# Kernel tuning notes

Measured on AMD Instinct MI355X. Metric: run time of the kernel, lower is better.

The kernel has to match this reference:

```python
import jax, jax.numpy as jnp
import numpy as np


def _rotate_half(x):
    x1, x2 = jnp.split(x, 2, axis=-1)
    return jnp.concatenate([-x2, x1], axis=-1)


def _rope_tables(seq_len, head_dim, base=10000.0):
    inv_freq = 1.0 / (base ** (jnp.arange(0, head_dim, 2, dtype=jnp.float32) / head_dim))
    t = jnp.arange(seq_len, dtype=jnp.float32)
    freqs = jnp.outer(t, inv_freq)  # [S, head_dim/2]
    # torch .repeat(...,2) tiles along last dim -> concat
    cos = jnp.concatenate([jnp.cos(freqs), jnp.cos(freqs)], axis=-1)  # [S, head_dim]
    sin = jnp.concatenate([jnp.sin(freqs), jnp.sin(freqs)], axis=-1)
    return cos[None, None], sin[None, None]  # [1,1,S,head_dim]


def setup_inputs() -> dict:
    key = jax.random.key(0)
    ks = jax.random.split(key, 5)
    B, S, D = 2, 2048, 2048
    sd = 1.0 / np.sqrt(D)
    return {
        "x": jax.random.normal(ks[0], (B, S, D), dtype=jnp.float32),
        "Wq": jax.random.normal(ks[1], (D, D), dtype=jnp.float32) * sd,
        "Wk": jax.random.normal(ks[2], (D, D), dtype=jnp.float32) * sd,
        "Wv": jax.random.normal(ks[3], (D, D), dtype=jnp.float32) * sd,
        "Wo": jax.random.normal(ks[4], (D, D), dtype=jnp.float32) * sd,
        "n_heads": 16,
    }


def reference(x, Wq, Wk, Wv, Wo, n_heads):
    B, S, D = x.shape
    hd = D // n_heads
    # projections (torch Linear: x @ W.T)
    def proj(W):
        return (x @ W.T).reshape(B, S, n_heads, hd).transpose(0, 2, 1, 3)  # [B,H,S,hd]
    q, k, v = proj(Wq), proj(Wk), proj(Wv)
    cos, sin = _rope_tables(S, hd)
    q = q * cos + _rotate_half(q) * sin
    k = k * cos + _rotate_half(k) * sin
    scale = 1.0 / np.sqrt(hd)
    scores = jnp.einsum('bhsd,bhtd->bhst', q, k) * scale  # [B,H,S,S]
    causal = jnp.triu(jnp.ones((S, S), dtype=bool), k=1)
    scores = jnp.where(causal[None, None], -jnp.inf, scores)
    attn = jax.nn.softmax(scores, axis=-1)
    out = jnp.einsum('bhst,bhtd->bhsd', attn, v)
    out = out.transpose(0, 2, 1, 3).reshape(B, S, D)
    return out @ Wo.T
```

## Files before the change

kernel.cpp:

```cpp
#include <hip/hip_runtime.h>
#include <hip/hip_bf16.h>
#include <math.h>

typedef __attribute__((ext_vector_type(8))) short bf16x8;
typedef __attribute__((ext_vector_type(4))) float f32x4;

#define GLB_CAST(p) ((const __attribute__((address_space(1))) void*)(p))
#define LDS_CAST(p) ((__attribute__((address_space(3))) void*)(p))

static __device__ __forceinline__ unsigned short bf16_bits(float x) {
    __hip_bfloat16 h = __float2bfloat16(x);
    return *(unsigned short*)&h;
}

__global__ void cvt_all(const float* __restrict__ x,  const float* __restrict__ wq,
                        const float* __restrict__ wk, const float* __restrict__ wv,
                        const float* __restrict__ wo,
                        __hip_bfloat16* __restrict__ xb,  __hip_bfloat16* __restrict__ wqb,
                        __hip_bfloat16* __restrict__ wkb, __hip_bfloat16* __restrict__ wvb,
                        __hip_bfloat16* __restrict__ wob)
{
    const size_t NX = 8388608, NW = 4194304;
    size_t i = ((size_t)blockIdx.x * 256 + threadIdx.x) * 8;
    const float* s; __hip_bfloat16* d; size_t off;
    if (i < NX) { s = x; d = xb; off = i; }
    else {
        size_t k = i - NX;
        const int seg = (int)(k >> 22);
        off = k & (NW - 1);
        s = seg == 0 ? wq : seg == 1 ? wk : seg == 2 ? wv : wo;
        d = seg == 0 ? wqb : seg == 1 ? wkb : seg == 2 ? wvb : wob;
    }
    float4 a = *(const float4*)(s + off);
    float4 b = *(const float4*)(s + off + 4);
    float t[8] = {a.x, a.y, a.z, a.w, b.x, b.y, b.z, b.w};
    union { unsigned short u[8]; uint4 v; } o;
#pragma unroll
    for (int j = 0; j < 8; ++j) o.u[j] = bf16_bits(t[j]);
    *(uint4*)(d + off) = o.v;
}

__global__ __launch_bounds__(256, 2)
void gemm_qkv(const __hip_bfloat16* __restrict__ A,
              const __hip_bfloat16* __restrict__ Wq,
              const __hip_bfloat16* __restrict__ Wk,
              const __hip_bfloat16* __restrict__ Wv,
              __hip_bfloat16* __restrict__ Qo,
              __hip_bfloat16* __restrict__ Ko,
              __hip_bfloat16* __restrict__ Vto)
{
    const int K = 2048;
    __shared__ __hip_bfloat16 As[128 * 32];
    __shared__ __hip_bfloat16 Bs[128 * 32];
    const int tid = threadIdx.x;
    const int w = tid >> 6, l = tid & 63;
    const int sel = blockIdx.y >> 4;
    const __hip_bfloat16* Bt = sel == 0 ? Wq : (sel == 1 ? Wk : Wv);
    const int m0 = blockIdx.x * 128, n0 = (blockIdx.y & 15) * 128;
    const int wr = w >> 1, wc = w & 1;
    const int lr = l & 15, kh = l >> 4;

    f32x4 acc[4][4] = {};

    for (int kt = 0; kt < 64; ++kt) {
        const int kb = kt * 32;
#pragma unroll
        for (int i = 0; i < 2; ++i) {
            const int s = i * 256 + tid;
            const int r = s >> 2, ks = (s & 3) * 8;
            __builtin_amdgcn_global_load_lds(GLB_CAST(A + (size_t)(m0 + r) * K + kb + ks),
                                             LDS_CAST(As + (size_t)(i * 256 + w * 64) * 8),
                                             16, 0, 0);
            __builtin_amdgcn_global_load_lds(GLB_CAST(Bt + (size_t)(n0 + r) * K + kb + ks),
                                             LDS_CAST(Bs + (size_t)(i * 256 + w * 64) * 8),
                                             16, 0, 0);
        }
        __syncthreads();
        bf16x8 af[4], bfr[4];
#pragma unroll
        for (int m = 0; m < 4; ++m)
            af[m] = *(const bf16x8*)(As + (wr * 64 + m * 16 + lr) * 32 + kh * 8);
#pragma unroll
        for (int n = 0; n < 4; ++n)
            bfr[n] = *(const bf16x8*)(Bs + (wc * 64 + n * 16 + lr) * 32 + kh * 8);
#pragma unroll
        for (int m = 0; m < 4; ++m)
#pragma unroll
            for (int n = 0; n < 4; ++n)
                acc[m][n] = __builtin_amdgcn_mfma_f32_16x16x32_bf16(af[m], bfr[n], acc[m][n], 0, 0, 0);
        __syncthreads();
    }

    __hip_bfloat16* Cout = sel == 0 ? Qo : (sel == 1 ? Ko : Vto);
#pragma unroll
    for (int m = 0; m < 4; ++m) {
        const int r0 = m0 + wr * 64 + m * 16 + kh * 4;
#pragma unroll
        for (int n = 0; n < 4; ++n) {
            const int c = n0 + wc * 64 + n * 16 + lr;
#pragma unroll
            for (int j = 0; j < 4; ++j) {
                const int r = r0 + j;
                const float v = acc[m][n][j];
                const int b = r >> 11, sy = r & 2047, h = c >> 7, dd = c & 127;
                if (sel < 2)
                    Cout[((size_t)(b * 16 + h) * 2048 + sy) * 128 + dd] = __float2bfloat16(v);
                else
                    Cout[((size_t)(b * 16 + h) * 128 + dd) * 2048 + sy] = __float2bfloat16(v);
            }
        }
    }
}

__global__ __launch_bounds__(256, 2)
void gemm_o(const __hip_bfloat16* __restrict__ A,
            const __hip_bfloat16* __restrict__ Bt,
            float* __restrict__ Cout)
{
    const int K = 2048;
    __shared__ __hip_bfloat16 As[128 * 32];
    __shared__ __hip_bfloat16 Bs[128 * 32];
    const int tid = threadIdx.x;
    const int w = tid >> 6, l = tid & 63;
    const int m0 = blockIdx.x * 128, n0 = blockIdx.y * 128;
    const int wr = w >> 1, wc = w & 1;
    const int lr = l & 15, kh = l >> 4;

    f32x4 acc[4][4] = {};

    for (int kt = 0; kt < 64; ++kt) {
        const int kb = kt * 32;
#pragma unroll
        for (int i = 0; i < 2; ++i) {
            const int s = i * 256 + tid;
            const int r = s >> 2, ks = (s & 3) * 8;
            __builtin_amdgcn_global_load_lds(GLB_CAST(A + (size_t)(m0 + r) * K + kb + ks),
                                             LDS_CAST(As + (size_t)(i * 256 + w * 64) * 8),
                                             16, 0, 0);
            __builtin_amdgcn_global_load_lds(GLB_CAST(Bt + (size_t)(n0 + r) * K + kb + ks),
                                             LDS_CAST(Bs + (size_t)(i * 256 + w * 64) * 8),
                                             16, 0, 0);
        }
        __syncthreads();
        bf16x8 af[4], bfr[4];
#pragma unroll
        for (int m = 0; m < 4; ++m)
            af[m] = *(const bf16x8*)(As + (wr * 64 + m * 16 + lr) * 32 + kh * 8);
#pragma unroll
        for (int n = 0; n < 4; ++n)
            bfr[n] = *(const bf16x8*)(Bs + (wc * 64 + n * 16 + lr) * 32 + kh * 8);
#pragma unroll
        for (int m = 0; m < 4; ++m)
#pragma unroll
            for (int n = 0; n < 4; ++n)
                acc[m][n] = __builtin_amdgcn_mfma_f32_16x16x32_bf16(af[m], bfr[n], acc[m][n], 0, 0, 0);
        __syncthreads();
    }

#pragma unroll
    for (int m = 0; m < 4; ++m) {
        const int r0 = m0 + wr * 64 + m * 16 + kh * 4;
#pragma unroll
        for (int n = 0; n < 4; ++n) {
            const int c = n0 + wc * 64 + n * 16 + lr;
#pragma unroll
            for (int j = 0; j < 4; ++j)
                Cout[(size_t)(r0 + j) * 2048 + c] = acc[m][n][j];
        }
    }
}

__global__ void rope_qk(__hip_bfloat16* __restrict__ Q, __hip_bfloat16* __restrict__ Kk) {
    const int row = blockIdx.x * 4 + (threadIdx.x >> 6);
    const int j = threadIdx.x & 63;
    const int s = row & 2047;
    const float inv = __expf((float)j * (-0.14391156831212787f));
    float sn, c;
    __sincosf((float)s * inv, &sn, &c);
    const size_t base = (size_t)row * 128;
    float q1 = __bfloat162float(Q[base + j]);
    float q2 = __bfloat162float(Q[base + 64 + j]);
    Q[base + j]      = __float2bfloat16(q1 * c - q2 * sn);
    Q[base + 64 + j] = __float2bfloat16(q2 * c + q1 * sn);
    float k1 = __bfloat162float(Kk[base + j]);
    float k2 = __bfloat162float(Kk[base + 64 + j]);
    Kk[base + j]      = __float2bfloat16(k1 * c - k2 * sn);
    Kk[base + 64 + j] = __float2bfloat16(k2 * c + k1 * sn);
}

__global__ __launch_bounds__(256, 3)
void flash_part(const __hip_bfloat16* __restrict__ Q,
                const __hip_bfloat16* __restrict__ K,
                const __hip_bfloat16* __restrict__ Vt,
                __hip_bfloat16* __restrict__ AO,
                __hip_bfloat16* __restrict__ OP,
                float* __restrict__ ML)
{
    const int bh = blockIdx.x;
    const int u  = blockIdx.y;
    const int tid = threadIdx.x, w = tid >> 6, l = tid & 63;
    const int lr = l & 15, hi = l >> 4;

    int G, part, P;
    if (u < 16)      { G = 12 + (u >> 2);            part = u & 3;   P = 4; }
    else if (u < 28) { int v = u - 16; G = 8 + v / 3; part = v % 3;  P = 3; }
    else if (u < 36) { int v = u - 28; G = 4 + (v >> 1); part = v & 1; P = 2; }
    else             { G = u - 36;                   part = 0;       P = 1; }
    const int nt = 4 * G + 4;
    const int t0 = (part * nt) / P, t1 = ((part + 1) * nt) / P;
    const bool split = (P > 1);
    const int qb = G * 128 + w * 32;
    const int q0 = qb + lr, q1 = qb + 16 + lr;

    const __hip_bfloat16* Qb = Q  + (size_t)bh * 2048 * 128;
    const __hip_bfloat16* Kb = K  + (size_t)bh * 2048 * 128;
    const __hip_bfloat16* Vb = Vt + (size_t)bh * 128 * 2048;

    __shared__ __align__(16) __hip_bfloat16 Ks[2][32 * 128];
    __shared__ __align__(16) __hip_bfloat16 Vs[2][128 * 32];

    bf16x8 qf[2][4];
#pragma unroll
    for (int g = 0; g < 2; ++g)
#pragma unroll
        for (int kk = 0; kk < 4; ++kk)
            qf[g][kk] = *(const bf16x8*)(Qb + (size_t)(qb + g * 16 + lr) * 128 + kk * 32 + hi * 8);

    int rK[2], cK[2], rV[2], cV[2];
#pragma unroll
    for (int i = 0; i < 2; ++i) {
        const int ci = i * 4 + w;
        rK[i] = ci * 4 + (l >> 4);
        cK[i] = ((l & 15) ^ (rK[i] & 7)) * 8;
        rV[i] = ci * 16 + (l >> 2);
        cV[i] = ((l & 3) ^ (rV[i] & 3)) * 8;
    }
    const int rsw7 = lr & 7, vsw3 = lr & 3;
    const int sA = lr + ((hi & 1) << 5);
    const int sB = sA + 16;
    const bool plo = (hi < 2);

#define STAGE(buf, t)                                                                        \
    {                                                                                        \
        const int kv0_ = (t) * 32;                                                           \
        _Pragma("unroll")                                                                    \
        for (int i = 0; i < 2; ++i) {                                                        \
            __builtin_amdgcn_global_load_lds(                                                \
                GLB_CAST(Kb + (size_t)(kv0_ + rK[i]) * 128 + cK[i]),                         \
                LDS_CAST(&Ks[buf][(i * 4 + w) * 512]), 16, 0, 0);                            \
            __builtin_amdgcn_global_load_lds(                                                \
                GLB_CAST(Vb + (size_t)rV[i] * 2048 + kv0_ + cV[i]),                          \
                LDS_CAST(&Vs[buf][(i * 4 + w) * 512]), 16, 0, 0);                            \
        }                                                                                    \
    }

    f32x4 o[2][8] = {};
    float mrow[2] = {-1e30f, -1e30f};
    float lrow[2] = {0.f, 0.f};
    const float scale = 0.08838834764831845f;

    int cur = 0;
    STAGE(0, t0);
    __syncthreads();

    for (int t = t0; t < t1; ++t) {
        if (t + 1 < t1) STAGE(cur ^ 1, t + 1);
        const __hip_bfloat16* Kc = &Ks[cur][0];
        const __hip_bfloat16* Vc = &Vs[cur][0];
        const int kv0 = t * 32;

        f32x4 sT[2][2] = {};
#pragma unroll
        for (int f = 0; f < 2; ++f)
#pragma unroll
            for (int kk = 0; kk < 4; ++kk) {
                const bf16x8 kf = *(const bf16x8*)(Kc + (f * 16 + lr) * 128 +
                                                   ((kk * 4 + hi) ^ rsw7) * 8);
                sT[0][f] = __builtin_amdgcn_mfma_f32_16x16x32_bf16(kf, qf[0][kk], sT[0][f], 0, 0, 0);
                sT[1][f] = __builtin_amdgcn_mfma_f32_16x16x32_bf16(kf, qf[1][kk], sT[1][f], 0, 0, 0);
            }

        float pmax[2] = {-1e30f, -1e30f};
#pragma unroll
        for (int g = 0; g < 2; ++g) {
            const int qown = g ? q1 : q0;
#pragma unroll
            for (int f = 0; f < 2; ++f)
#pragma unroll
                for (int j = 0; j < 4; ++j) {
                    const int kv = kv0 + f * 16 + hi * 4 + j;
                    float v = sT[g][f][j] * scale;
                    v = (kv > qown) ? -1e30f : v;
                    sT[g][f][j] = v;
                    pmax[g] = fmaxf(pmax[g], v);
                }
            pmax[g] = fmaxf(pmax[g], __shfl_xor(pmax[g], 16));
            pmax[g] = fmaxf(pmax[g], __shfl_xor(pmax[g], 32));
        }

        if (!__all(pmax[0] <= mrow[0] + 8.f && pmax[1] <= mrow[1] + 8.f)) {
#pragma unroll
            for (int g = 0; g < 2; ++g) {
                const float mnew = fmaxf(mrow[g], pmax[g]);
                const float alpha = __expf(mrow[g] - mnew);
                mrow[g] = mnew;
                lrow[g] *= alpha;
                float aj[4];
#pragma unroll
                for (int j = 0; j < 4; ++j)
                    aj[j] = __shfl(alpha, (l & 48) | (hi * 4 + j), 64);
#pragma unroll
                for (int dn = 0; dn < 8; ++dn)
#pragma unroll
                    for (int j = 0; j < 4; ++j) o[g][dn][j] *= aj[j];
            }
        }

#pragma unroll
        for (int g = 0; g < 2; ++g) {
            float rs = 0.f;
#pragma unroll
            for (int f = 0; f < 2; ++f)
#pragma unroll
                for (int j = 0; j < 4; ++j) {
                    const float pv = __expf(sT[g][f][j] - mrow[g]);
                    sT[g][f][j] = pv;
                    rs += pv;
                }
            rs += __shfl_xor(rs, 16);
            rs += __shfl_xor(rs, 32);
            lrow[g] += rs;
        }

        union { unsigned u[4]; bf16x8 v; } pf[2];
#pragma unroll
        for (int g = 0; g < 2; ++g) {
            unsigned wds[4];
#pragma unroll
            for (int i = 0; i < 4; ++i)
                wds[i] = (unsigned)bf16_bits(sT[g][i >> 1][(i & 1) * 2]) |
                         ((unsigned)bf16_bits(sT[g][i >> 1][(i & 1) * 2 + 1]) << 16);
            const unsigned a0 = __shfl((int)wds[0], sA, 64), a1 = __shfl((int)wds[1], sA, 64);
            const unsigned a2 = __shfl((int)wds[2], sA, 64), a3 = __shfl((int)wds[3], sA, 64);
            const unsigned b0 = __shfl((int)wds[0], sB, 64), b1 = __shfl((int)wds[1], sB, 64);
            const unsigned b2 = __shfl((int)wds[2], sB, 64), b3 = __shfl((int)wds[3], sB, 64);
            pf[g].u[0] = plo ? a0 : a2;
            pf[g].u[1] = plo ? a1 : a3;
            pf[g].u[2] = plo ? b0 : b2;
            pf[g].u[3] = plo ? b1 : b3;
        }

#pragma unroll
        for (int dn = 0; dn < 8; ++dn) {
            const bf16x8 vf = *(const bf16x8*)(Vc + (dn * 16 + lr) * 32 + (hi ^ vsw3) * 8);
            o[0][dn] = __builtin_amdgcn_mfma_f32_16x16x32_bf16(pf[0].v, vf, o[0][dn], 0, 0, 0);
            o[1][dn] = __builtin_amdgcn_mfma_f32_16x16x32_bf16(pf[1].v, vf, o[1][dn], 0, 0, 0);
        }
        __syncthreads();
        cur ^= 1;
    }
#undef STAGE

    if (!split) {
#pragma unroll
        for (int g = 0; g < 2; ++g) {
            float linv[4];
#pragma unroll
            for (int j = 0; j < 4; ++j)
                linv[j] = 1.0f / __shfl(lrow[g], (l & 48) | (hi * 4 + j), 64);
#pragma unroll
            for (int j = 0; j < 4; ++j) {
                const int q = qb + g * 16 + hi * 4 + j;
                const size_t rb = ((size_t)(bh >> 4) * 2048 + q) * 2048 + (size_t)(bh & 15) * 128;
#pragma unroll
                for (int dn = 0; dn < 8; ++dn)
                    AO[rb + dn * 16 + lr] = __float2bfloat16(o[g][dn][j] * linv[j]);
            }
        }
    } else {
        const int base = (G < 8) ? (G - 4) * 2 : ((G < 12) ? 8 + (G - 8) * 3
                                                           : 20 + (G - 12) * 4);
        const int pidx = bh * 36 + base + part;
#pragma unroll
        for (int g = 0; g < 2; ++g) {
#pragma unroll
            for (int j = 0; j < 4; ++j) {
                const int row = w * 32 + g * 16 + hi * 4 + j;
#pragma unroll
                for (int dn = 0; dn < 8; ++dn)
                    OP[((size_t)pidx * 128 + row) * 128 + dn * 16 + lr] =
                        __float2bfloat16(o[g][dn][j]);
            }
            if (l < 16) {
                const int row = w * 32 + g * 16 + l;
                ML[((size_t)pidx * 128 + row) * 2]     = mrow[g];
                ML[((size_t)pidx * 128 + row) * 2 + 1] = lrow[g];
            }
        }
    }
}

__global__ void flash_merge(const __hip_bfloat16* __restrict__ OP,
                            const float* __restrict__ ML,
                            __hip_bfloat16* __restrict__ AO)
{
    const int gi = blockIdx.x % 12, bh = blockIdx.x / 12;
    const int G = 4 + gi;
    const int P = (G < 8) ? 2 : ((G < 12) ? 3 : 4);
    const int base = (G < 8) ? (G - 4) * 2 : ((G < 12) ? 8 + (G - 8) * 3
                                                       : 20 + (G - 12) * 4);
    const int pidx0 = bh * 36 + base;
    const int t = threadIdx.x, r = t >> 1, c0 = (t & 1) * 64;

    float m[4], lv[4];
    float M = -1e30f;
#pragma unroll
    for (int p = 0; p < 4; ++p) if (p < P) {
        m[p]  = ML[((size_t)(pidx0 + p) * 128 + r) * 2];
        lv[p] = ML[((size_t)(pidx0 + p) * 128 + r) * 2 + 1];
        M = fmaxf(M, m[p]);
    }
    float wgt[4];
    float den = 0.f;
#pragma unroll
    for (int p = 0; p < 4; ++p) if (p < P) {
        wgt[p] = __expf(m[p] - M);
        den += lv[p] * wgt[p];
    }
    const float inv = 1.0f / den;

    const int q = G * 128 + r;
    __hip_bfloat16* out = AO + ((size_t)(bh >> 4) * 2048 + q) * 2048 + (size_t)(bh & 15) * 128 + c0;

#pragma unroll
    for (int ch = 0; ch < 8; ++ch) {
        float acc[8] = {0.f, 0.f, 0.f, 0.f, 0.f, 0.f, 0.f, 0.f};
#pragma unroll
        for (int p = 0; p < 4; ++p) if (p < P) {
            const bf16x8 v = *(const bf16x8*)(OP + ((size_t)(pidx0 + p) * 128 + r) * 128 + c0 + ch * 8);
#pragma unroll
            for (int i = 0; i < 8; ++i) {
                __hip_bfloat16 hv;
                *(short*)&hv = v[i];
                acc[i] += __bfloat162float(hv) * wgt[p];
            }
        }
        union { unsigned short us[8]; bf16x8 v; } rr;
#pragma unroll
        for (int i = 0; i < 8; ++i) rr.us[i] = bf16_bits(acc[i] * inv);
        *(bf16x8*)(out + ch * 8) = rr.v;
    }
}

extern "C" void kernel_launch(void* const* d_in, const int* in_sizes, int n_in,
                              void* d_out, int out_size, void* d_ws, size_t ws_size,
                              hipStream_t stream) {
    (void)in_sizes; (void)n_in; (void)out_size; (void)ws_size;
    const float* x  = (const float*)d_in[0];
    const float* Wq = (const float*)d_in[1];
    const float* Wk = (const float*)d_in[2];
    const float* Wv = (const float*)d_in[3];
    const float* Wo = (const float*)d_in[4];

    char* p = (char*)d_ws;
    auto carve = [&](size_t bytes) -> char* {
        char* r = p;
        p += (bytes + 255) & ~(size_t)255;
        return r;
    };
    __hip_bfloat16* xb  = (__hip_bfloat16*)carve(4096ull * 2048 * 2);
    __hip_bfloat16* Wqb = (__hip_bfloat16*)carve(2048ull * 2048 * 2);
    __hip_bfloat16* Wkb = (__hip_bfloat16*)carve(2048ull * 2048 * 2);
    __hip_bfloat16* Wvb = (__hip_bfloat16*)carve(2048ull * 2048 * 2);
    __hip_bfloat16* Wob = (__hip_bfloat16*)carve(2048ull * 2048 * 2);
    __hip_bfloat16* Qb  = (__hip_bfloat16*)carve(32ull * 2048 * 128 * 2);
    __hip_bfloat16* Kb  = (__hip_bfloat16*)carve(32ull * 2048 * 128 * 2);
    __hip_bfloat16* Vtb = (__hip_bfloat16*)carve(32ull * 128 * 2048 * 2);
    __hip_bfloat16* OPb = (__hip_bfloat16*)carve(32ull * 36 * 128 * 128 * 2);
    float*          MLb = (float*)carve(32ull * 36 * 128 * 2 * 4);

    cvt_all<<<12288, 256, 0, stream>>>(x, Wq, Wk, Wv, Wo, xb, Wqb, Wkb, Wvb, Wob);

    gemm_qkv<<<dim3(32, 48), 256, 0, stream>>>(xb, Wqb, Wkb, Wvb, Qb, Kb, Vtb);

    rope_qk<<<16384, 256, 0, stream>>>(Qb, Kb);

    flash_part<<<dim3(32, 40), 256, 0, stream>>>(Qb, Kb, Vtb, xb , OPb, MLb);
    flash_merge<<<384, 256, 0, stream>>>(OPb, MLb, xb );

    gemm_o<<<dim3(32, 16), 256, 0, stream>>>(xb, Wob, (float*)d_out);
}
```

Measured before the change: 323.1 us.

## Rewrite QKV GEMM with 256x256 tiles, double-buffered swizzled LDS and staged MFMA

Replaces the 128x128, single-buffered QKV projection GEMM with a 256x256-tile, 512-thread kernel using a K-step of 64. Global-to-LDS loads are double-buffered and interleaved with four MFMA quadrants under explicit barriers and priority hints. An XOR swizzle is applied to the LDS layout to avoid bank conflicts. This aims to raise reuse per byte loaded and hide memory latency behind compute, at the cost of heavy LDS use (128KB), more registers, and fewer blocks (384) on the device.

```diff
diff --git a/kernel.cpp b/kernel.cpp
--- a/kernel.cpp
+++ b/kernel.cpp
@@ -40,69 +40,150 @@
     *(uint4*)(d + off) = o.v;
 }
 
-__global__ __launch_bounds__(256, 2)
-void gemm_qkv(const __hip_bfloat16* __restrict__ A,
-              const __hip_bfloat16* __restrict__ Wq,
-              const __hip_bfloat16* __restrict__ Wk,
-              const __hip_bfloat16* __restrict__ Wv,
-              __hip_bfloat16* __restrict__ Qo,
-              __hip_bfloat16* __restrict__ Ko,
-              __hip_bfloat16* __restrict__ Vto)
+__global__ __launch_bounds__(512, 2)
+void gemm_qkv256(const __hip_bfloat16* __restrict__ A,
+                 const __hip_bfloat16* __restrict__ Wq,
+                 const __hip_bfloat16* __restrict__ Wk,
+                 const __hip_bfloat16* __restrict__ Wv,
+                 __hip_bfloat16* __restrict__ Qo,
+                 __hip_bfloat16* __restrict__ Ko,
+                 __hip_bfloat16* __restrict__ Vto)
 {
-    const int K = 2048;
-    __shared__ __hip_bfloat16 As[128 * 32];
-    __shared__ __hip_bfloat16 Bs[128 * 32];
+    const int K = 2048, NT = 32;
+    __shared__ __align__(16) __hip_bfloat16 As[2][16384];
+    __shared__ __align__(16) __hip_bfloat16 Bs[2][16384];
     const int tid = threadIdx.x;
     const int w = tid >> 6, l = tid & 63;
-    const int sel = blockIdx.y >> 4;
+    const int lr = l & 15, hi = l >> 4;
+    const int wm = w >> 2, wn = w & 3;
+    const int sel = blockIdx.y >> 3;
     const __hip_bfloat16* Bt = sel == 0 ? Wq : (sel == 1 ? Wk : Wv);
-    const int m0 = blockIdx.x * 128, n0 = (blockIdx.y & 15) * 128;
-    const int wr = w >> 1, wc = w & 1;
-    const int lr = l & 15, kh = l >> 4;
-
-    f32x4 acc[4][4] = {};
-
-    for (int kt = 0; kt < 64; ++kt) {
-        const int kb = kt * 32;
-#pragma unroll
-        for (int i = 0; i < 2; ++i) {
-            const int s = i * 256 + tid;
-            const int r = s >> 2, ks = (s & 3) * 8;
-            __builtin_amdgcn_global_load_lds(GLB_CAST(A + (size_t)(m0 + r) * K + kb + ks),
-                                             LDS_CAST(As + (size_t)(i * 256 + w * 64) * 8),
-                                             16, 0, 0);
-            __builtin_amdgcn_global_load_lds(GLB_CAST(Bt + (size_t)(n0 + r) * K + kb + ks),
-                                             LDS_CAST(Bs + (size_t)(i * 256 + w * 64) * 8),
-                                             16, 0, 0);
-        }
-        __syncthreads();
-        bf16x8 af[4], bfr[4];
+    const int m0 = blockIdx.x * 256, n0 = (blockIdx.y & 7) * 256;
+
+    const int sw0 = (hi ^ (lr & 7)) * 8;
+    const int sw1 = ((hi ^ (lr & 7)) ^ 4) * 8;
+
+#define BARS() { __builtin_amdgcn_s_barrier(); __builtin_amdgcn_sched_barrier(0); }
+#define STAGE_A(b, t, h)                                                                     \
+    { _Pragma("unroll") for (int r_ = 0; r_ < 2; ++r_) {                                     \
+        const int slot_ = r_ * 512 + tid;                                                    \
+        const int row_ = (h) * 128 + (slot_ >> 3);                                           \
+        const int sc_ = ((slot_ & 7) ^ (row_ & 7)) * 8;                                      \
+        __builtin_amdgcn_global_load_lds(                                                    \
+            GLB_CAST(A + (size_t)(m0 + row_) * K + (t) * 64 + sc_),                          \
+            LDS_CAST(&As[b][((h) * 1024 + r_ * 512 + w * 64) * 8]), 16, 0, 0); } }
+#define STAGE_B(b, t, h)                                                                     \
+    { _Pragma("unroll") for (int r_ = 0; r_ < 2; ++r_) {                                     \
+        const int slot_ = r_ * 512 + tid;                                                    \
+        const int row_ = (h) * 128 + (slot_ >> 3);                                           \
+        const int sc_ = ((slot_ & 7) ^ (row_ & 7)) * 8;                                      \
+        __builtin_amdgcn_global_load_lds(                                                    \
+            GLB_CAST(Bt + (size_t)(n0 + row_) * K + (t) * 64 + sc_),                         \
+            LDS_CAST(&Bs[b][((h) * 1024 + r_ * 512 + w * 64) * 8]), 16, 0, 0); } }
+
+    f32x4 acc[8][4] = {};
+
+    STAGE_A(0, 0, 0); STAGE_A(0, 0, 1); STAGE_B(0, 0, 0); STAGE_B(0, 0, 1);
+    STAGE_B(1, 1, 0); STAGE_B(1, 1, 1);
+    asm volatile("s_waitcnt vmcnt(0)" ::: "memory");
+    BARS();
+
+    for (int t = 0; t < NT; ++t) {
+        const int cur = t & 1;
+        const __hip_bfloat16* Ac = &As[cur][(wm * 128 + lr) * 64];
+        const __hip_bfloat16* Bc = &Bs[cur][(wn * 64 + lr) * 64];
+        bf16x8 aR[4][2], aS[4][2], bR[2][2], bS[2][2];
+
+#pragma unroll
+        for (int m = 0; m < 4; ++m) {
+            aR[m][0] = *(const bf16x8*)(Ac + m * 1024 + sw0);
+            aR[m][1] = *(const bf16x8*)(Ac + m * 1024 + sw1);
+        }
+#pragma unroll
+        for (int n = 0; n < 2; ++n) {
+            bR[n][0] = *(const bf16x8*)(Bc + n * 1024 + sw0);
+            bR[n][1] = *(const bf16x8*)(Bc + n * 1024 + sw1);
+        }
+        if (t + 1 < NT) STAGE_A(cur ^ 1, t + 1, 0);
+        BARS();
+        __builtin_amdgcn_s_setprio(1);
 #pragma unroll
         for (int m = 0; m < 4; ++m)
-            af[m] = *(const bf16x8*)(As + (wr * 64 + m * 16 + lr) * 32 + kh * 8);
-#pragma unroll
-        for (int n = 0; n < 4; ++n)
-            bfr[n] = *(const bf16x8*)(Bs + (wc * 64 + n * 16 + lr) * 32 + kh * 8);
+#pragma unroll
+            for (int n = 0; n < 2; ++n) {
+                acc[m][n] = __builtin_amdgcn_mfma_f32_16x16x32_bf16(aR[m][0], bR[n][0], acc[m][n], 0, 0, 0);
+                acc[m][n] = __builtin_amdgcn_mfma_f32_16x16x32_bf16(aR[m][1], bR[n][1], acc[m][n], 0, 0, 0);
+            }
+        __builtin_amdgcn_s_setprio(0);
+        BARS();
+
+#pragma unroll
+        for (int n = 0; n < 2; ++n) {
+            bS[n][0] = *(const bf16x8*)(Bc + (2 + n) * 1024 + sw0);
+            bS[n][1] = *(const bf16x8*)(Bc + (2 + n) * 1024 + sw1);
+        }
+        if (t + 1 < NT) STAGE_A(cur ^ 1, t + 1, 1);
+        BARS();
+        __builtin_amdgcn_s_setprio(1);
 #pragma unroll
         for (int m = 0; m < 4; ++m)
 #pragma unroll
-            for (int n = 0; n < 4; ++n)
-                acc[m][n] = __builtin_amdgcn_mfma_f32_16x16x32_bf16(af[m], bfr[n], acc[m][n], 0, 0, 0);
-        __syncthreads();
-    }
+            for (int n = 0; n < 2; ++n) {
+                acc[m][2 + n] = __builtin_amdgcn_mfma_f32_16x16x32_bf16(aR[m][0], bS[n][0], acc[m][2 + n], 0, 0, 0);
+                acc[m][2 + n] = __builtin_amdgcn_mfma_f32_16x16x32_bf16(aR[m][1], bS[n][1], acc[m][2 + n], 0, 0, 0);
+            }
+        __builtin_amdgcn_s_setprio(0);
+        BARS();
+
+#pragma unroll
+        for (int m = 0; m < 4; ++m) {
+            aS[m][0] = *(const bf16x8*)(Ac + (4 + m) * 1024 + sw0);
+            aS[m][1] = *(const bf16x8*)(Ac + (4 + m) * 1024 + sw1);
+        }
+        if (t + 2 < NT) STAGE_B(cur, t + 2, 0);
+        BARS();
+        __builtin_amdgcn_s_setprio(1);
+#pragma unroll
+        for (int m = 0; m < 4; ++m)
+#pragma unroll
+            for (int n = 0; n < 2; ++n) {
+                acc[4 + m][2 + n] = __builtin_amdgcn_mfma_f32_16x16x32_bf16(aS[m][0], bS[n][0], acc[4 + m][2 + n], 0, 0, 0);
+                acc[4 + m][2 + n] = __builtin_amdgcn_mfma_f32_16x16x32_bf16(aS[m][1], bS[n][1], acc[4 + m][2 + n], 0, 0, 0);
+            }
+        __builtin_amdgcn_s_setprio(0);
+        BARS();
+
+        if (t + 2 < NT) STAGE_B(cur, t + 2, 1);
+        asm volatile("s_waitcnt vmcnt(4)" ::: "memory");
+        BARS();
+        __builtin_amdgcn_s_setprio(1);
+#pragma unroll
+        for (int m = 0; m < 4; ++m)
+#pragma unroll
+            for (int n = 0; n < 2; ++n) {
+                acc[4 + m][n] = __builtin_amdgcn_mfma_f32_16x16x32_bf16(aS[m][0], bR[n][0], acc[4 + m][n], 0, 0, 0);
+                acc[4 + m][n] = __builtin_amdgcn_mfma_f32_16x16x32_bf16(aS[m][1], bR[n][1], acc[4 + m][n], 0, 0, 0);
+            }
+        __builtin_amdgcn_s_setprio(0);
+        BARS();
+    }
+#undef STAGE_A
+#undef STAGE_B
+#undef BARS
 
     __hip_bfloat16* Cout = sel == 0 ? Qo : (sel == 1 ? Ko : Vto);
 #pragma unroll
-    for (int m = 0; m < 4; ++m) {
-        const int r0 = m0 + wr * 64 + m * 16 + kh * 4;
+    for (int m = 0; m < 8; ++m) {
+        const int r0 = m0 + wm * 128 + m * 16 + hi * 4;
 #pragma unroll
         for (int n = 0; n < 4; ++n) {
-            const int c = n0 + wc * 64 + n * 16 + lr;
+            const int c = n0 + wn * 64 + n * 16 + lr;
+            const int h = c >> 7, dd = c & 127;
 #pragma unroll
             for (int j = 0; j < 4; ++j) {
                 const int r = r0 + j;
+                const int b = r >> 11, sy = r & 2047;
                 const float v = acc[m][n][j];
-                const int b = r >> 11, sy = r & 2047, h = c >> 7, dd = c & 127;
                 if (sel < 2)
                     Cout[((size_t)(b * 16 + h) * 2048 + sy) * 128 + dd] = __float2bfloat16(v);
                 else
@@ -481,7 +562,7 @@
 
     cvt_all<<<12288, 256, 0, stream>>>(x, Wq, Wk, Wv, Wo, xb, Wqb, Wkb, Wvb, Wob);
 
-    gemm_qkv<<<dim3(32, 48), 256, 0, stream>>>(xb, Wqb, Wkb, Wvb, Qb, Kb, Vtb);
+    gemm_qkv256<<<dim3(16, 24), 512, 0, stream>>>(xb, Wqb, Wkb, Wvb, Qb, Kb, Vtb);
 
     rope_qk<<<16384, 256, 0, stream>>>(Qb, Kb);
 
```

Result: slower. 337.9 us (+4.6%).
